# Performance work log

Hardware: AMD Instinct MI355X
Metric: run time of the kernel (lower is better)

## Reference

```python
import jax, jax.numpy as jnp
import numpy as np


def setup_inputs() -> dict:
    key = jax.random.key(0)
    ks = jax.random.split(key, 7)
    C, V, D, B = 8, 12, 64, 32768
    return {
        "idx": jax.random.randint(ks[0], (C, B), 0, V),
        "label": jax.random.uniform(ks[1], (B, 2), dtype=jnp.float32),
        "pos_weights": jax.random.uniform(ks[2], (B, 2), dtype=jnp.float32),
        "mean_table": jax.random.normal(ks[3], (C, V, D), dtype=jnp.float32),
        "std_table": jax.random.normal(ks[4], (C, V, D), dtype=jnp.float32),
        "action_table": jax.random.normal(ks[5], (2, D), dtype=jnp.float32),
        "noise": jax.random.normal(ks[6], (B * D,), dtype=jnp.float32),
    }


def reference(idx, label, pos_weights, mean_table, std_table, action_table, noise):
    C, B = idx.shape
    D = mean_table.shape[-1]
    cols = jnp.arange(C)[:, None]                       # [C,1]
    mu = mean_table[cols, idx]                          # [C,B,D] gather
    std = jax.nn.softplus(std_table[cols, idx])         # log(1+exp(.)) == softplus
    # NOTE: torch slices the SAME rand_array prefix for every reparameterize
    # call, so the noise is shared across all columns.
    v = noise[: B * D].reshape(1, B, D)
    e = mu + std * v * 0.01                             # [C,B,D] reparameterized embeddings
    s = e.sum(axis=0)                                   # [B,D]
    # sum_{i<j} <e_i, e_j> = 0.5*(||sum_i e_i||^2 - sum_i ||e_i||^2)
    # (computed then discarded by torch forward; exposed here as 3rd output)
    pairwise = 0.5 * ((s * s).sum(-1) - (e * e).sum(axis=(0, -1)))[:, None]  # [B,1]
    inf0 = s @ action_table[0]                          # [B]
    inf1 = s @ action_table[1]                          # [B]
    inferences = jnp.stack([inf0, inf1], axis=1)        # [B,2]
    loss = (inferences - label) ** 2
    weighted_loss = jnp.mean(jnp.sum(pos_weights * loss, axis=1))
    return inferences, weighted_loss, pairwise
```

## Files before the change

kernel.cpp:

```cpp
#include <hip/hip_runtime.h>
#include <math.h>

#define NC 8
#define NV 12
#define ND 64
#define NB 32768
#define NROWS 96
#define RSW 68
#define OUT_LOSS 65536
#define OUT_PW   65537

__device__ __forceinline__ unsigned bf16rne(float x) {
    const unsigned u = __float_as_uint(x);
    return (u + 0x7FFFu + ((u >> 16) & 1u)) >> 16;
}

__device__ __forceinline__ float fast_softplus(float x) {
    const float t = __builtin_exp2f(x * 1.44269504f);
    return 0.69314718f * __builtin_log2f(1.0f + t);
}

__global__ __launch_bounds__(1024, 4) void fm_main(
    const int*   __restrict__ idx,
    const float* __restrict__ label,
    const float* __restrict__ posw,
    const float* __restrict__ meant,
    const float* __restrict__ stdt,
    const float* __restrict__ act,
    const float* __restrict__ noise,
    float*       __restrict__ out,
    float*       __restrict__ partial)
{
    __shared__ unsigned tab[NROWS * RSW];
    __shared__ float wloss[16];

    const int tid  = threadIdx.x;
    const int lane = tid & 63;
    const int wave = tid >> 6;
    const int m    = lane & 7;
    const int bsub = lane >> 3;
    const int b    = blockIdx.x * 128 + wave * 8 + bsub;

    int g[NC];
    #pragma unroll
    for (int c = 0; c < NC; ++c) g[c] = idx[c * NB + b];

    const float4 vl = *(const float4*)(noise + b * ND + 8*m);
    const float4 vh = *(const float4*)(noise + b * ND + 8*m + 4);

    const float4 a0l = *(const float4*)(act + 8*m);
    const float4 a0h = *(const float4*)(act + 8*m + 4);
    const float4 a1l = *(const float4*)(act + ND + 8*m);
    const float4 a1h = *(const float4*)(act + ND + 8*m + 4);

    float2 lb = make_float2(0.f, 0.f), pw = make_float2(0.f, 0.f);
    if (m == 0) {
        lb = *(const float2*)(label + 2*b);
        pw = *(const float2*)(posw + 2*b);
    }

    for (int i = tid * 4; i < NROWS * ND; i += 1024 * 4) {
        const float4 mu4 = *(const float4*)(meant + i);
        const float4 sd4 = *(const float4*)(stdt + i);
        const int r = i >> 6, d = i & 63;
        uint4 w;
        w.x = bf16rne(mu4.x) | (bf16rne(fast_softplus(sd4.x) * 0.01f) << 16);
        w.y = bf16rne(mu4.y) | (bf16rne(fast_softplus(sd4.y) * 0.01f) << 16);
        w.z = bf16rne(mu4.z) | (bf16rne(fast_softplus(sd4.z) * 0.01f) << 16);
        w.w = bf16rne(mu4.w) | (bf16rne(fast_softplus(sd4.w) * 0.01f) << 16);
        *(uint4*)(&tab[r * RSW + d]) = w;
    }
    __syncthreads();

    float s0=0,s1=0,s2=0,s3=0,s4=0,s5=0,s6=0,s7=0;
    float esq = 0.f;

    #pragma unroll
    for (int c = 0; c < NC; ++c) {
        const unsigned* rp = &tab[(c * NV + g[c]) * RSW + 8*m];
        const uint4 w0 = *(const uint4*)(rp);
        const uint4 w1 = *(const uint4*)(rp + 4);
#define EMB(W, VV, SS) { \
        const float mu_ = __uint_as_float((W) << 16); \
        const float sp_ = __uint_as_float((W) & 0xFFFF0000u); \
        const float e_  = fmaf(sp_, (VV), mu_); \
        SS += e_; esq = fmaf(e_, e_, esq); }
        EMB(w0.x, vl.x, s0) EMB(w0.y, vl.y, s1) EMB(w0.z, vl.z, s2) EMB(w0.w, vl.w, s3)
        EMB(w1.x, vh.x, s4) EMB(w1.y, vh.y, s5) EMB(w1.z, vh.z, s6) EMB(w1.w, vh.w, s7)
#undef EMB
    }

    float r0 = s0*s0+s1*s1+s2*s2+s3*s3+s4*s4+s5*s5+s6*s6+s7*s7;
    float r1 = esq;
    float r2 = s0*a0l.x+s1*a0l.y+s2*a0l.z+s3*a0l.w+s4*a0h.x+s5*a0h.y+s6*a0h.z+s7*a0h.w;
    float r3 = s0*a1l.x+s1*a1l.y+s2*a1l.z+s3*a1l.w+s4*a1h.x+s5*a1h.y+s6*a1h.z+s7*a1h.w;

    #pragma unroll
    for (int off = 1; off <= 4; off <<= 1) {
        r0 += __shfl_xor(r0, off, 64);
        r1 += __shfl_xor(r1, off, 64);
        r2 += __shfl_xor(r2, off, 64);
        r3 += __shfl_xor(r3, off, 64);
    }

    float lossacc = 0.f;
    if (m == 0) {
        ((float2*)out)[b] = make_float2(r2, r3);
        out[OUT_PW + b]   = 0.5f * (r0 - r1);
        const float d0 = r2 - lb.x, d1 = r3 - lb.y;
        lossacc = pw.x*d0*d0 + pw.y*d1*d1;
    }

    #pragma unroll
    for (int off = 8; off <= 32; off <<= 1) lossacc += __shfl_xor(lossacc, off, 64);
    if (lane == 0) wloss[wave] = lossacc;
    __syncthreads();
    if (tid == 0) {
        float s = 0.f;
        #pragma unroll
        for (int i = 0; i < 16; ++i) s += wloss[i];
        partial[blockIdx.x] = s;
    }
}

__global__ __launch_bounds__(256) void fm_loss(const float* __restrict__ partial,
                                               float* __restrict__ out) {
    const int tid = threadIdx.x;
    float v = partial[tid];
    #pragma unroll
    for (int off = 1; off <= 32; off <<= 1) v += __shfl_xor(v, off, 64);
    __shared__ float ws[4];
    if ((tid & 63) == 0) ws[tid >> 6] = v;
    __syncthreads();
    if (tid == 0) out[OUT_LOSS] = (ws[0]+ws[1]+ws[2]+ws[3]) * (1.0f/(float)NB);
}

extern "C" void kernel_launch(void* const* d_in, const int* in_sizes, int n_in,
                              void* d_out, int out_size, void* d_ws, size_t ws_size,
                              hipStream_t stream) {
    const int*   idx   = (const int*)d_in[0];
    const float* label = (const float*)d_in[1];
    const float* posw  = (const float*)d_in[2];
    const float* meant = (const float*)d_in[3];
    const float* stdt  = (const float*)d_in[4];
    const float* act   = (const float*)d_in[5];
    const float* noise = (const float*)d_in[6];
    float* out = (float*)d_out;
    float* partial = (float*)d_ws;

    fm_main<<<256, 1024, 0, stream>>>(idx, label, posw, meant, stdt, act, noise, out, partial);
    fm_loss<<<1, 256, 0, stream>>>(partial, out);
}
```

Before: 12.51 us.

## Split table staging into two halves overlapping packing with gather

Table loads for the mean and std tables are now issued at kernel start, before the index and noise loads, so their latency overlaps. The packing of the 96-row table is split: threads 0-383 pack columns 0-3, then a barrier, and threads 384-767 pack columns 4-7 while all threads gather columns 0-3, with a second barrier before gathering columns 4-7. The final loss kernel shrinks to one wave using float4 loads and no shared memory. This adds an extra block barrier and leaves packing work unevenly spread across threads.

Result: no change. 12.73 us (+1.8%).

```diff
diff --git a/kernel.cpp b/kernel.cpp
--- a/kernel.cpp
+++ b/kernel.cpp
@@ -41,6 +41,15 @@
     const int bsub = lane >> 3;
     const int b    = blockIdx.x * 128 + wave * 8 + bsub;
 
+    float4 muA, muB, sdA, sdB;
+    const int si = tid * 8;
+    if (tid < 768) {
+        muA = *(const float4*)(meant + si);
+        muB = *(const float4*)(meant + si + 4);
+        sdA = *(const float4*)(stdt + si);
+        sdB = *(const float4*)(stdt + si + 4);
+    }
+
     int g[NC];
     #pragma unroll
     for (int c = 0; c < NC; ++c) g[c] = idx[c * NB + b];
@@ -59,36 +68,46 @@
         pw = *(const float2*)(posw + 2*b);
     }
 
-    for (int i = tid * 4; i < NROWS * ND; i += 1024 * 4) {
-        const float4 mu4 = *(const float4*)(meant + i);
-        const float4 sd4 = *(const float4*)(stdt + i);
-        const int r = i >> 6, d = i & 63;
-        uint4 w;
-        w.x = bf16rne(mu4.x) | (bf16rne(fast_softplus(sd4.x) * 0.01f) << 16);
-        w.y = bf16rne(mu4.y) | (bf16rne(fast_softplus(sd4.y) * 0.01f) << 16);
-        w.z = bf16rne(mu4.z) | (bf16rne(fast_softplus(sd4.z) * 0.01f) << 16);
-        w.w = bf16rne(mu4.w) | (bf16rne(fast_softplus(sd4.w) * 0.01f) << 16);
-        *(uint4*)(&tab[r * RSW + d]) = w;
-    }
+#define PACKROW() { \
+        const int r = si >> 6, d = si & 63; \
+        uint4 wA, wB; \
+        wA.x = bf16rne(muA.x) | (bf16rne(fast_softplus(sdA.x) * 0.01f) << 16); \
+        wA.y = bf16rne(muA.y) | (bf16rne(fast_softplus(sdA.y) * 0.01f) << 16); \
+        wA.z = bf16rne(muA.z) | (bf16rne(fast_softplus(sdA.z) * 0.01f) << 16); \
+        wA.w = bf16rne(muA.w) | (bf16rne(fast_softplus(sdA.w) * 0.01f) << 16); \
+        wB.x = bf16rne(muB.x) | (bf16rne(fast_softplus(sdB.x) * 0.01f) << 16); \
+        wB.y = bf16rne(muB.y) | (bf16rne(fast_softplus(sdB.y) * 0.01f) << 16); \
+        wB.z = bf16rne(muB.z) | (bf16rne(fast_softplus(sdB.z) * 0.01f) << 16); \
+        wB.w = bf16rne(muB.w) | (bf16rne(fast_softplus(sdB.w) * 0.01f) << 16); \
+        *(uint4*)(&tab[r * RSW + d])     = wA; \
+        *(uint4*)(&tab[r * RSW + d + 4]) = wB; }
+
+    if (tid < 384) PACKROW();
     __syncthreads();
+
+    if (tid >= 384 && tid < 768) PACKROW();
+#undef PACKROW
 
     float s0=0,s1=0,s2=0,s3=0,s4=0,s5=0,s6=0,s7=0;
     float esq = 0.f;
 
-    #pragma unroll
-    for (int c = 0; c < NC; ++c) {
-        const unsigned* rp = &tab[(c * NV + g[c]) * RSW + 8*m];
-        const uint4 w0 = *(const uint4*)(rp);
-        const uint4 w1 = *(const uint4*)(rp + 4);
 #define EMB(W, VV, SS) { \
         const float mu_ = __uint_as_float((W) << 16); \
         const float sp_ = __uint_as_float((W) & 0xFFFF0000u); \
         const float e_  = fmaf(sp_, (VV), mu_); \
         SS += e_; esq = fmaf(e_, e_, esq); }
-        EMB(w0.x, vl.x, s0) EMB(w0.y, vl.y, s1) EMB(w0.z, vl.z, s2) EMB(w0.w, vl.w, s3)
-        EMB(w1.x, vh.x, s4) EMB(w1.y, vh.y, s5) EMB(w1.z, vh.z, s6) EMB(w1.w, vh.w, s7)
+#define GATHER(C) { \
+        const unsigned* rp = &tab[((C) * NV + g[(C)]) * RSW + 8*m]; \
+        const uint4 w0 = *(const uint4*)(rp); \
+        const uint4 w1 = *(const uint4*)(rp + 4); \
+        EMB(w0.x, vl.x, s0) EMB(w0.y, vl.y, s1) EMB(w0.z, vl.z, s2) EMB(w0.w, vl.w, s3) \
+        EMB(w1.x, vh.x, s4) EMB(w1.y, vh.y, s5) EMB(w1.z, vh.z, s6) EMB(w1.w, vh.w, s7) }
+
+    GATHER(0) GATHER(1) GATHER(2) GATHER(3)
+    __syncthreads();
+    GATHER(4) GATHER(5) GATHER(6) GATHER(7)
+#undef GATHER
 #undef EMB
-    }
 
     float r0 = s0*s0+s1*s1+s2*s2+s3*s3+s4*s4+s5*s5+s6*s6+s7*s7;
     float r1 = esq;
@@ -123,16 +142,14 @@
     }
 }
 
-__global__ __launch_bounds__(256) void fm_loss(const float* __restrict__ partial,
-                                               float* __restrict__ out) {
-    const int tid = threadIdx.x;
-    float v = partial[tid];
+__global__ __launch_bounds__(64) void fm_loss(const float* __restrict__ partial,
+                                              float* __restrict__ out) {
+    const int lane = threadIdx.x;
+    const float4 p = *(const float4*)(partial + lane * 4);
+    float v = (p.x + p.y) + (p.z + p.w);
     #pragma unroll
     for (int off = 1; off <= 32; off <<= 1) v += __shfl_xor(v, off, 64);
-    __shared__ float ws[4];
-    if ((tid & 63) == 0) ws[tid >> 6] = v;
-    __syncthreads();
-    if (tid == 0) out[OUT_LOSS] = (ws[0]+ws[1]+ws[2]+ws[3]) * (1.0f/(float)NB);
+    if (lane == 0) out[OUT_LOSS] = v * (1.0f / (float)NB);
 }
 
 extern "C" void kernel_launch(void* const* d_in, const int* in_sizes, int n_in,
@@ -149,5 +166,5 @@
     float* partial = (float*)d_ws;
 
     fm_main<<<256, 1024, 0, stream>>>(idx, label, posw, meant, stdt, act, noise, out, partial);
-    fm_loss<<<1, 256, 0, stream>>>(partial, out);
+    fm_loss<<<1, 64, 0, stream>>>(partial, out);
 }
```
